# Optimization experiments

Measured on AMD Instinct MI355X. Metric: run time of the kernel, lower is better.

The kernel has to match this reference:

```python
import jax, jax.numpy as jnp
import numpy as np
import math

B, S, H, NH, NKV, D, I, LCK = 2, 1024, 2048, 32, 8, 64, 8192, 3
EPS = 1e-6
THETA = 10000.0


def rms_norm(x, w, eps=EPS):
    xf = x.astype(jnp.float32)
    var = jnp.mean(xf * xf, axis=-1, keepdims=True)
    return (w * (xf * jax.lax.rsqrt(var + eps))).astype(x.dtype)


def rotate_half(x):
    d = x.shape[-1] // 2
    return jnp.concatenate([-x[..., d:], x[..., :d]], axis=-1)


def setup_inputs() -> dict:
    key = jax.random.key(0)
    ks = jax.random.split(key, 16)
    sc = 0.02
    inp = {
        'input_emb': jax.random.normal(ks[0], (B, S, H), jnp.float32),
        'hidden_states': jax.random.normal(ks[1], (B, S, H), jnp.float32),
        'cache_k': jax.random.normal(ks[2], (LCK, B, NH, S, D), jnp.float32),
        'cache_v': jax.random.normal(ks[3], (LCK, B, NH, S, D), jnp.float32),
    }
    neg = jnp.finfo(jnp.float32).min
    causal = jnp.where(jnp.tril(jnp.ones((S, S), bool)), 0.0, neg).astype(jnp.float32)
    inp['attention_mask'] = jnp.broadcast_to(causal[None, None], (B, 1, S, S))
    inp['position_ids'] = jnp.broadcast_to(jnp.arange(S, dtype=jnp.int32)[None], (B, S))
    inp['wq'] = jax.random.normal(ks[4], (NH * D, 2 * H), jnp.float32) * sc
    inp['wk'] = jax.random.normal(ks[5], (NKV * D, 2 * H), jnp.float32) * sc
    inp['wv'] = jax.random.normal(ks[6], (NKV * D, 2 * H), jnp.float32) * sc
    inp['wo'] = jax.random.normal(ks[7], (H, NH * D), jnp.float32) * sc
    inp['w_gate'] = jax.random.normal(ks[8], (I, H), jnp.float32) * sc
    inp['w_up'] = jax.random.normal(ks[9], (I, H), jnp.float32) * sc
    inp['w_down'] = jax.random.normal(ks[10], (H, I), jnp.float32) * sc
    inp['hidden_norm_w'] = jnp.ones((H,), jnp.float32)
    inp['input_ln_w'] = jnp.ones((H,), jnp.float32)
    inp['post_ln_w'] = jnp.ones((H,), jnp.float32)
    return inp


def _forward(input_emb, hidden_states, cache_k, cache_v, attention_mask, position_ids,
             wq, wk, wv, wo, w_gate, w_up, w_down, hidden_norm_w, input_ln_w, post_ln_w):
    residual = hidden_states
    h = rms_norm(hidden_states, hidden_norm_w)
    e = rms_norm(input_emb, input_ln_w)
    x = jnp.concatenate([e, h], axis=-1)  # [B,S,2H]

    q = jnp.einsum('bsi,oi->bso', x, wq).reshape(B, S, NH, D).transpose(0, 2, 1, 3)
    k = jnp.einsum('bsi,oi->bso', x, wk).reshape(B, S, NKV, D).transpose(0, 2, 1, 3)
    v = jnp.einsum('bsi,oi->bso', x, wv).reshape(B, S, NKV, D).transpose(0, 2, 1, 3)

    # RoPE table up to seq_len = S + LCK, indexed at position_ids + LCK
    inv_freq = 1.0 / (THETA ** (jnp.arange(0, D, 2, dtype=jnp.float32) / D))
    t = jnp.arange(S + LCK, dtype=jnp.float32)
    freqs = t[:, None] * inv_freq[None, :]
    emb = jnp.concatenate([freqs, freqs], axis=-1)  # [S+LCK, D]
    pos = position_ids + LCK
    cos = jnp.cos(emb)[pos][:, None]  # [B,1,S,D]
    sin = jnp.sin(emb)[pos][:, None]
    q = q * cos + rotate_half(q) * sin
    k = k * cos + rotate_half(k) * sin

    n_rep = NH // NKV
    k = jnp.repeat(k, n_rep, axis=1)  # [B,NH,S,D]
    v = jnp.repeat(v, n_rep, axis=1)

    scale = 1.0 / math.sqrt(D)
    # full causal attention against the oldest cache entry
    s0 = jnp.einsum('bhqd,bhkd->bhqk', q, cache_k[0]) * scale + attention_mask
    # diagonal (same-position) attention against remaining cache entries + current keys
    extra_k = jnp.concatenate([cache_k[1:], k[None]], axis=0)  # [LCK,B,NH,S,D]
    extra_v = jnp.concatenate([cache_v[1:], v[None]], axis=0)
    sd = jnp.einsum('bhqd,nbhqd->bhqn', q, extra_k) * scale  # [B,NH,S,LCK]

    attn = jax.nn.softmax(jnp.concatenate([s0, sd], axis=-1).astype(jnp.float32), axis=-1).astype(q.dtype)
    out = jnp.einsum('bhqk,bhkd->bhqd', attn[..., :S], cache_v[0])
    out = out + jnp.einsum('bhqn,nbhqd->bhqd', attn[..., S:], extra_v)
    out = out.transpose(0, 2, 1, 3).reshape(B, S, NH * D)
    attn_out = jnp.einsum('bsi,oi->bso', out, wo)

    h2 = residual + attn_out
    hn = rms_norm(h2, post_ln_w)
    mlp = jnp.einsum('bsi,oi->bso', jax.nn.silu(jnp.einsum('bsi,oi->bso', hn, w_gate)) * jnp.einsum('bsi,oi->bso', hn, w_up), w_down)
    return h2 + mlp


def reference(input_emb, hidden_states, cache_k, cache_v, attention_mask, position_ids,
              wq, wk, wv, wo, w_gate, w_up, w_down, hidden_norm_w, input_ln_w, post_ln_w):
    return _forward(input_emb, hidden_states, cache_k, cache_v, attention_mask, position_ids,
                    wq, wk, wv, wo, w_gate, w_up, w_down, hidden_norm_w, input_ln_w, post_ln_w)
```

## Files before the change

kernel.cpp:

```cpp
#include <hip/hip_runtime.h>
#include <math.h>

#define B_   2
#define S_   1024
#define H_   2048
#define NH_  32
#define NKV_ 8
#define D_   64
#define I_   8192
#define LCK_ 3
#define M_   (B_ * S_)

typedef unsigned short u16;
typedef unsigned int   u32;
typedef __attribute__((ext_vector_type(8))) short bf16x8;
typedef __attribute__((ext_vector_type(4))) float f32x4;
typedef __attribute__((ext_vector_type(2))) unsigned int u32x2;

__device__ __forceinline__ u16 f2b(float f) {
  u32 u = __float_as_uint(f);
  u += 0x7fffu + ((u >> 16) & 1u);
  return (u16)(u >> 16);
}
__device__ __forceinline__ float b2f(u16 h) { return __uint_as_float(((u32)h) << 16); }

__device__ __forceinline__ void st_bf4(u16* p, float a, float b, float c, float d) {
  u32x2 v;
  v.x = (u32)f2b(a) | ((u32)f2b(b) << 16);
  v.y = (u32)f2b(c) | ((u32)f2b(d) << 16);
  *(u32x2*)p = v;
}

__device__ __forceinline__ void cvt16(const float4& a, const float4& b,
                                      const float4& c, const float4& d,
                                      bf16x8& lo, bf16x8& hi) {
  lo[0] = (short)f2b(a.x); lo[1] = (short)f2b(a.y); lo[2] = (short)f2b(a.z); lo[3] = (short)f2b(a.w);
  lo[4] = (short)f2b(b.x); lo[5] = (short)f2b(b.y); lo[6] = (short)f2b(b.z); lo[7] = (short)f2b(b.w);
  hi[0] = (short)f2b(c.x); hi[1] = (short)f2b(c.y); hi[2] = (short)f2b(c.z); hi[3] = (short)f2b(c.w);
  hi[4] = (short)f2b(d.x); hi[5] = (short)f2b(d.y); hi[6] = (short)f2b(d.z); hi[7] = (short)f2b(d.w);
}

__device__ __forceinline__ void async16(const void* g, void* l) {
  __builtin_amdgcn_global_load_lds(
      (const __attribute__((address_space(1))) unsigned int*)(uintptr_t)g,
      (__attribute__((address_space(3))) unsigned int*)(unsigned int)(uintptr_t)l,
      16, 0, 0);
}

__global__ __launch_bounds__(256) void norm_concat_kernel(
    const float* __restrict__ emb, const float* __restrict__ hid,
    const float* __restrict__ w_e, const float* __restrict__ w_h,
    u16* __restrict__ x)
{
  const int row = blockIdx.x;
  const int t = threadIdx.x;
  const float* e = emb + (size_t)row * H_;
  const float* h = hid + (size_t)row * H_;

  const float4 ev0 = *(const float4*)&e[t * 4];
  const float4 ev1 = *(const float4*)&e[t * 4 + 1024];
  const float4 hv0 = *(const float4*)&h[t * 4];
  const float4 hv1 = *(const float4*)&h[t * 4 + 1024];

  float se = ev0.x*ev0.x + ev0.y*ev0.y + ev0.z*ev0.z + ev0.w*ev0.w
           + ev1.x*ev1.x + ev1.y*ev1.y + ev1.z*ev1.z + ev1.w*ev1.w;
  float sh = hv0.x*hv0.x + hv0.y*hv0.y + hv0.z*hv0.z + hv0.w*hv0.w
           + hv1.x*hv1.x + hv1.y*hv1.y + hv1.z*hv1.z + hv1.w*hv1.w;

  #pragma unroll
  for (int m = 1; m < 64; m <<= 1) {
    se += __shfl_xor(se, m);
    sh += __shfl_xor(sh, m);
  }
  __shared__ float red[8];
  const int wv = t >> 6;
  if ((t & 63) == 0) { red[wv] = se; red[4 + wv] = sh; }
  __syncthreads();
  se = red[0] + red[1] + red[2] + red[3];
  sh = red[4] + red[5] + red[6] + red[7];

  const float re = 1.0f / sqrtf(se * (1.0f / H_) + 1e-6f);
  const float rh = 1.0f / sqrtf(sh * (1.0f / H_) + 1e-6f);

  const float4 we0 = *(const float4*)&w_e[t * 4];
  const float4 we1 = *(const float4*)&w_e[t * 4 + 1024];
  const float4 wh0 = *(const float4*)&w_h[t * 4];
  const float4 wh1 = *(const float4*)&w_h[t * 4 + 1024];

  u16* xr = x + (size_t)row * (2 * H_);
  st_bf4(&xr[t * 4],        ev0.x*re*we0.x, ev0.y*re*we0.y, ev0.z*re*we0.z, ev0.w*re*we0.w);
  st_bf4(&xr[t * 4 + 1024], ev1.x*re*we1.x, ev1.y*re*we1.y, ev1.z*re*we1.z, ev1.w*re*we1.w);
  st_bf4(&xr[2048 + t * 4],        hv0.x*rh*wh0.x, hv0.y*rh*wh0.y, hv0.z*rh*wh0.z, hv0.w*rh*wh0.w);
  st_bf4(&xr[2048 + t * 4 + 1024], hv1.x*rh*wh1.x, hv1.y*rh*wh1.y, hv1.z*rh*wh1.z, hv1.w*rh*wh1.w);
}

__global__ __launch_bounds__(256) void rmsnorm_kernel(
    const float* __restrict__ in, const float* __restrict__ w, u16* __restrict__ outp)
{
  const int row = blockIdx.x;
  const int t = threadIdx.x;
  const float* p = in + (size_t)row * H_;
  const float4 v0 = *(const float4*)&p[t * 4];
  const float4 v1 = *(const float4*)&p[t * 4 + 1024];
  float s = v0.x*v0.x + v0.y*v0.y + v0.z*v0.z + v0.w*v0.w
          + v1.x*v1.x + v1.y*v1.y + v1.z*v1.z + v1.w*v1.w;
  #pragma unroll
  for (int m = 1; m < 64; m <<= 1) s += __shfl_xor(s, m);
  __shared__ float red[4];
  const int wv = t >> 6;
  if ((t & 63) == 0) red[wv] = s;
  __syncthreads();
  s = red[0] + red[1] + red[2] + red[3];
  const float rs = 1.0f / sqrtf(s * (1.0f / H_) + 1e-6f);

  const float4 w0 = *(const float4*)&w[t * 4];
  const float4 w1 = *(const float4*)&w[t * 4 + 1024];
  u16* orow = outp + (size_t)row * H_;
  st_bf4(&orow[t * 4],        v0.x*rs*w0.x, v0.y*rs*w0.y, v0.z*rs*w0.z, v0.w*rs*w0.w);
  st_bf4(&orow[t * 4 + 1024], v1.x*rs*w1.x, v1.y*rs*w1.y, v1.z*rs*w1.z, v1.w*rs*w1.w);
}

__global__ __launch_bounds__(256) void convert6_kernel(
    const float* __restrict__ wq, const float* __restrict__ wk, const float* __restrict__ wv,
    const float* __restrict__ wo, const float* __restrict__ wg, const float* __restrict__ wu,
    u16* __restrict__ dst)
{
  const size_t i8 = ((size_t)blockIdx.x * 256 + threadIdx.x) * 8;
  const float* s; size_t base;
  if      (i8 <  8388608) { s = wq; base = 0; }
  else if (i8 < 10485760) { s = wk; base = 8388608; }
  else if (i8 < 12582912) { s = wv; base = 10485760; }
  else if (i8 < 16777216) { s = wo; base = 12582912; }
  else if (i8 < 33554432) { s = wg; base = 16777216; }
  else                    { s = wu; base = 33554432; }
  const float4 a = *(const float4*)&s[i8 - base];
  const float4 b = *(const float4*)&s[i8 - base + 4];
  bf16x8 r;
  r[0] = (short)f2b(a.x); r[1] = (short)f2b(a.y); r[2] = (short)f2b(a.z); r[3] = (short)f2b(a.w);
  r[4] = (short)f2b(b.x); r[5] = (short)f2b(b.y); r[6] = (short)f2b(b.z); r[7] = (short)f2b(b.w);
  *(bf16x8*)&dst[i8] = r;
}

__global__ __launch_bounds__(256) void convert1_kernel(
    const float* __restrict__ src, u16* __restrict__ dst)
{
  const size_t i8 = ((size_t)blockIdx.x * 256 + threadIdx.x) * 8;
  const float4 a = *(const float4*)&src[i8];
  const float4 b = *(const float4*)&src[i8 + 4];
  bf16x8 r;
  r[0] = (short)f2b(a.x); r[1] = (short)f2b(a.y); r[2] = (short)f2b(a.z); r[3] = (short)f2b(a.w);
  r[4] = (short)f2b(b.x); r[5] = (short)f2b(b.y); r[6] = (short)f2b(b.z); r[7] = (short)f2b(b.w);
  *(bf16x8*)&dst[i8] = r;
}

template <int MODE>
__global__ __launch_bounds__(256) void gemm_bf16_kernel(
    const u16* __restrict__ A, const u16* __restrict__ Bw,
    void* Cv, const void* Xv, int M, int N, int K)
{
  __shared__ __align__(16) u16 As[128 * 32];
  __shared__ __align__(16) u16 Bs[128 * 32];
  const int t = threadIdx.x;
  const int lane = t & 63;
  const int w = t >> 6;
  const int wr = w >> 1, wc = w & 1;
  const int row0 = blockIdx.y * 128;
  const int col0 = blockIdx.x * 128;
  const int kz = blockIdx.z;
  const int Kc = K / (int)gridDim.z;

  f32x4 acc[4][4];
  #pragma unroll
  for (int i = 0; i < 4; ++i)
    #pragma unroll
    for (int j = 0; j < 4; ++j)
      #pragma unroll
      for (int r = 0; r < 4; ++r) acc[i][j][r] = 0.f;

  const int srow = lane >> 2;
  const int skc  = (lane & 3) * 8;
  const u16* Ag = A  + (size_t)(row0 + w * 32 + srow) * K + skc + (size_t)kz * Kc;
  const u16* Bg = Bw + (size_t)(col0 + w * 32 + srow) * K + skc + (size_t)kz * Kc;
  u16* AsW = &As[w * 32 * 32];
  u16* BsW = &Bs[w * 32 * 32];

  const int fr = lane & 15;
  const int fq = (lane >> 4) * 8;

  for (int k0 = 0; k0 < Kc; k0 += 32) {
    __syncthreads();
    async16(Ag + k0,                  AsW);
    async16(Ag + k0 + (size_t)16 * K, AsW + 16 * 32);
    async16(Bg + k0,                  BsW);
    async16(Bg + k0 + (size_t)16 * K, BsW + 16 * 32);
    __syncthreads();

    bf16x8 af[4], bfr[4];
    #pragma unroll
    for (int ti = 0; ti < 4; ++ti)
      af[ti] = *(const bf16x8*)&As[(wr * 64 + ti * 16 + fr) * 32 + fq];
    #pragma unroll
    for (int tj = 0; tj < 4; ++tj)
      bfr[tj] = *(const bf16x8*)&Bs[(wc * 64 + tj * 16 + fr) * 32 + fq];
    #pragma unroll
    for (int ti = 0; ti < 4; ++ti)
      #pragma unroll
      for (int tj = 0; tj < 4; ++tj)
        acc[ti][tj] = __builtin_amdgcn_mfma_f32_16x16x32_bf16(af[ti], bfr[tj], acc[ti][tj], 0, 0, 0);
  }

  float* Cf = (float*)Cv + (size_t)kz * ((size_t)M * N);
  u16*  Cb = (u16*)Cv;
  const float* Xf = (const float*)Xv;
  const u16*  Xb = (const u16*)Xv;
  const int rbase = (lane >> 4) * 4;
  const int cofs  = lane & 15;
  #pragma unroll
  for (int ti = 0; ti < 4; ++ti) {
    #pragma unroll
    for (int r = 0; r < 4; ++r) {
      const int gr = row0 + wr * 64 + ti * 16 + rbase + r;
      #pragma unroll
      for (int tj = 0; tj < 4; ++tj) {
        const int gc = col0 + wc * 64 + tj * 16 + cofs;
        const size_t off = (size_t)gr * N + gc;
        const float v = acc[ti][tj][r];
        if constexpr (MODE == 0) {
          Cf[off] = v;
        } else if constexpr (MODE == 1) {
          Cf[off] = v + Xf[off];
        } else if constexpr (MODE == 2) {
          Cb[off] = f2b(v);
        } else {
          const float g = b2f(Xb[off]);
          Cb[off] = f2b((g / (1.f + __expf(-g))) * v);
        }
      }
    }
  }
}

template <int NP>
__global__ __launch_bounds__(256) void reduce_kernel(
    const float* __restrict__ p, const float* __restrict__ resid,
    float* __restrict__ out, size_t nper)
{
  const size_t i = ((size_t)blockIdx.x * 256 + threadIdx.x) * 4;
  float4 s = *(const float4*)&p[i];
  #pragma unroll
  for (int z = 1; z < NP; ++z) {
    const float4 a = *(const float4*)&p[(size_t)z * nper + i];
    s.x += a.x; s.y += a.y; s.z += a.z; s.w += a.w;
  }
  if (resid) {
    const float4 r = *(const float4*)&resid[i];
    s.x += r.x; s.y += r.y; s.z += r.z; s.w += r.w;
  }
  *(float4*)&out[i] = s;
}

__global__ __launch_bounds__(256) void rope_kernel(
    float* __restrict__ qkv, const int* __restrict__ pid)
{
  const int idx = blockIdx.x * 256 + threadIdx.x;
  const int total = M_ * (NH_ + NKV_) * 32;
  if (idx >= total) return;
  const int row = idx / 1280;
  const int rem = idx - row * 1280;
  const int head = rem >> 5;
  const int i = rem & 31;
  const int col = (head < NH_) ? head * 64 : 2048 + (head - NH_) * 64;
  float* base = qkv + (size_t)row * 3072 + col;
  const int pos = pid[row] + LCK_;
  const float invf = powf(10000.0f, -(float)i * (1.0f / 32.0f));
  const float ang = (float)pos * invf;
  const float c  = cosf(ang);
  const float sn = sinf(ang);
  const float x0 = base[i];
  const float x1 = base[i + 32];
  base[i]      = x0 * c - x1 * sn;
  base[i + 32] = x1 * c + x0 * sn;
}

__global__ __launch_bounds__(256) void attn_kernel(
    const float* __restrict__ qkv,
    const float* __restrict__ ck, const float* __restrict__ cv,
    u16* __restrict__ ao)
{
  const int bid = blockIdx.x;
  const int qt = bid & 15;
  const int bh = bid >> 4;
  const int h = bh & 31;
  const int b = bh >> 5;
  const int t = threadIdx.x;
  const int lane = t & 63;
  const int w = t >> 6;
  const int qbase = qt * 64;

  const int fr = lane & 15;
  const int fq = (lane >> 4) * 8;
  const int rbase = (lane >> 4) * 4;
  const int cofs = lane & 15;

  __shared__ __align__(16) u16 Qs[64 * 72];
  __shared__ __align__(16) u16 Ks[64 * 72];
  __shared__ __align__(16) u16 Vts[64 * 72];
  __shared__ __align__(16) u16 Ps[64 * 72];
  __shared__ float Ls[192];

  const size_t bh_off = (size_t)b * NH_ + h;
  const float* K0 = ck + bh_off * S_ * D_;
  const float* V0 = cv + bh_off * S_ * D_;

  const int sr = t >> 2;
  const int sc = (t & 3) * 16;
  {
    const float* qg = qkv + (size_t)(b * S_ + qbase + sr) * 3072 + h * 64 + sc;
    float4 a = *(const float4*)&qg[0], bb = *(const float4*)&qg[4],
           c = *(const float4*)&qg[8], d = *(const float4*)&qg[12];
    a.x*=0.125f; a.y*=0.125f; a.z*=0.125f; a.w*=0.125f;
    bb.x*=0.125f; bb.y*=0.125f; bb.z*=0.125f; bb.w*=0.125f;
    c.x*=0.125f; c.y*=0.125f; c.z*=0.125f; c.w*=0.125f;
    d.x*=0.125f; d.y*=0.125f; d.z*=0.125f; d.w*=0.125f;
    bf16x8 lo, hi; cvt16(a, bb, c, d, lo, hi);
    *(bf16x8*)&Qs[sr * 72 + sc] = lo;
    *(bf16x8*)&Qs[sr * 72 + sc + 8] = hi;
  }

  float m_r[4], l_r[4];
  f32x4 Oacc[4];
  #pragma unroll
  for (int r = 0; r < 4; ++r) { m_r[r] = -3.0e38f; l_r[r] = 0.f; }
  #pragma unroll
  for (int dt = 0; dt < 4; ++dt)
    #pragma unroll
    for (int r = 0; r < 4; ++r) Oacc[dt][r] = 0.f;

  for (int kt = 0; kt <= qt; ++kt) {
    __syncthreads();
    {
      const float* kg = K0 + (size_t)(kt * 64 + sr) * D_ + sc;
      float4 a = *(const float4*)&kg[0], bb = *(const float4*)&kg[4],
             c = *(const float4*)&kg[8], d = *(const float4*)&kg[12];
      bf16x8 lo, hi; cvt16(a, bb, c, d, lo, hi);
      *(bf16x8*)&Ks[sr * 72 + sc] = lo;
      *(bf16x8*)&Ks[sr * 72 + sc + 8] = hi;
      const float* vg = V0 + (size_t)(kt * 64 + sr) * D_ + sc;
      float4 va = *(const float4*)&vg[0], vb4 = *(const float4*)&vg[4],
             vc = *(const float4*)&vg[8], vd = *(const float4*)&vg[12];
      const float vv[16] = {va.x,va.y,va.z,va.w, vb4.x,vb4.y,vb4.z,vb4.w,
                            vc.x,vc.y,vc.z,vc.w, vd.x,vd.y,vd.z,vd.w};
      #pragma unroll
      for (int i = 0; i < 16; ++i) Vts[(sc + i) * 72 + sr] = f2b(vv[i]);
    }
    __syncthreads();

    const bf16x8 qa0 = *(const bf16x8*)&Qs[(w * 16 + fr) * 72 + fq];
    const bf16x8 qa1 = *(const bf16x8*)&Qs[(w * 16 + fr) * 72 + 32 + fq];
    f32x4 sacc[4];
    #pragma unroll
    for (int nt = 0; nt < 4; ++nt) {
      const bf16x8 kb0 = *(const bf16x8*)&Ks[(nt * 16 + fr) * 72 + fq];
      const bf16x8 kb1 = *(const bf16x8*)&Ks[(nt * 16 + fr) * 72 + 32 + fq];
      f32x4 z; z[0]=0.f; z[1]=0.f; z[2]=0.f; z[3]=0.f;
      z = __builtin_amdgcn_mfma_f32_16x16x32_bf16(qa0, kb0, z, 0, 0, 0);
      sacc[nt] = __builtin_amdgcn_mfma_f32_16x16x32_bf16(qa1, kb1, z, 0, 0, 0);
    }
    if (kt == qt) {
      #pragma unroll
      for (int nt = 0; nt < 4; ++nt) {
        const int key = nt * 16 + cofs;
        #pragma unroll
        for (int r = 0; r < 4; ++r)
          if (key > w * 16 + rbase + r) sacc[nt][r] = -3.0e38f;
      }
    }

    #pragma unroll
    for (int r = 0; r < 4; ++r) {
      float rm = fmaxf(fmaxf(sacc[0][r], sacc[1][r]), fmaxf(sacc[2][r], sacc[3][r]));
      rm = fmaxf(rm, __shfl_xor(rm, 1));
      rm = fmaxf(rm, __shfl_xor(rm, 2));
      rm = fmaxf(rm, __shfl_xor(rm, 4));
      rm = fmaxf(rm, __shfl_xor(rm, 8));
      const float mnew = fmaxf(m_r[r], rm);
      const float alpha = __expf(m_r[r] - mnew);
      float p0 = __expf(sacc[0][r] - mnew);
      float p1 = __expf(sacc[1][r] - mnew);
      float p2 = __expf(sacc[2][r] - mnew);
      float p3 = __expf(sacc[3][r] - mnew);
      float rs = p0 + p1 + p2 + p3;
      rs += __shfl_xor(rs, 1);
      rs += __shfl_xor(rs, 2);
      rs += __shfl_xor(rs, 4);
      rs += __shfl_xor(rs, 8);
      l_r[r] = l_r[r] * alpha + rs;
      m_r[r] = mnew;
      #pragma unroll
      for (int dt = 0; dt < 4; ++dt) Oacc[dt][r] *= alpha;
      u16* prow = &Ps[(w * 16 + rbase + r) * 72 + cofs];
      prow[0]  = f2b(p0);
      prow[16] = f2b(p1);
      prow[32] = f2b(p2);
      prow[48] = f2b(p3);
    }

    const bf16x8 pa0 = *(const bf16x8*)&Ps[(w * 16 + fr) * 72 + fq];
    const bf16x8 pa1 = *(const bf16x8*)&Ps[(w * 16 + fr) * 72 + 32 + fq];
    #pragma unroll
    for (int dt = 0; dt < 4; ++dt) {
      const bf16x8 vb0 = *(const bf16x8*)&Vts[(dt * 16 + fr) * 72 + fq];
      const bf16x8 vb1 = *(const bf16x8*)&Vts[(dt * 16 + fr) * 72 + 32 + fq];
      Oacc[dt] = __builtin_amdgcn_mfma_f32_16x16x32_bf16(pa0, vb0, Oacc[dt], 0, 0, 0);
      Oacc[dt] = __builtin_amdgcn_mfma_f32_16x16x32_bf16(pa1, vb1, Oacc[dt], 0, 0, 0);
    }
  }

  if (t < 192) {
    const int n = t >> 6;
    const int r = t & 63;
    const int qp = qbase + r;
    const float* kp;
    if (n < 2) kp = ck + ((((size_t)(n + 1) * B_ + b) * NH_ + h) * S_ + qp) * D_;
    else       kp = qkv + (size_t)(b * S_ + qp) * 3072 + 2048 + (h >> 2) * 64;
    float e = 0.f;
    #pragma unroll 16
    for (int d = 0; d < 64; ++d) e = fmaf(b2f(Qs[r * 72 + d]), kp[d], e);
    Ls[n * 64 + r] = e;
  }
  __syncthreads();

  #pragma unroll
  for (int r = 0; r < 4; ++r) {
    const int qr = w * 16 + rbase + r;
    const int qp = qbase + qr;
    const float e0 = Ls[qr], e1 = Ls[64 + qr], e2 = Ls[128 + qr];
    const float mnew = fmaxf(fmaxf(m_r[r], e0), fmaxf(e1, e2));
    const float alpha = __expf(m_r[r] - mnew);
    const float p0 = __expf(e0 - mnew);
    const float p1 = __expf(e1 - mnew);
    const float p2 = __expf(e2 - mnew);
    const float inv = 1.0f / (l_r[r] * alpha + p0 + p1 + p2);
    const float* v1p = cv + ((((size_t)1 * B_ + b) * NH_ + h) * S_ + qp) * D_;
    const float* v2p = cv + ((((size_t)2 * B_ + b) * NH_ + h) * S_ + qp) * D_;
    const float* v3p = qkv + (size_t)(b * S_ + qp) * 3072 + 2560 + (h >> 2) * 64;
    u16* aorow = ao + (size_t)(b * S_ + qp) * 2048 + h * 64;
    #pragma unroll
    for (int dt = 0; dt < 4; ++dt) {
      const int col = dt * 16 + cofs;
      const float o = (Oacc[dt][r] * alpha + p0 * v1p[col] + p1 * v2p[col] + p2 * v3p[col]) * inv;
      aorow[col] = f2b(o);
    }
  }
}

extern "C" void kernel_launch(void* const* d_in, const int* in_sizes, int n_in,
                              void* d_out, int out_size, void* d_ws, size_t ws_size,
                              hipStream_t stream)
{
  const float* input_emb = (const float*)d_in[0];
  const float* hidden    = (const float*)d_in[1];
  const float* cache_k   = (const float*)d_in[2];
  const float* cache_v   = (const float*)d_in[3];
  const int*   pos_ids   = (const int*)d_in[5];
  const float* wq = (const float*)d_in[6];
  const float* wk = (const float*)d_in[7];
  const float* wv = (const float*)d_in[8];
  const float* wo = (const float*)d_in[9];
  const float* wg = (const float*)d_in[10];
  const float* wu = (const float*)d_in[11];
  const float* wd = (const float*)d_in[12];
  const float* w_hidden_norm = (const float*)d_in[13];
  const float* w_input_ln    = (const float*)d_in[14];
  const float* w_post_ln     = (const float*)d_in[15];
  float* out = (float*)d_out;

  char* wsb = (char*)d_ws;
  u16*   wall   = (u16*)(wsb + 0);
  u16*   wqkv_b = wall;
  u16*   wo_b   = (u16*)(wsb + 25165824);
  u16*   wg_b   = (u16*)(wsb + 33554432);
  u16*   wu_b   = (u16*)(wsb + 67108864);
  u16*   xb     = (u16*)(wsb + 100663296);
  float* qkvf   = (float*)(wsb + 117440512);
  u16*   ao     = (u16*)(wsb + 142606336);
  float* h2     = (float*)(wsb + 150994944);
  u16*   hn     = (u16*)(wsb + 100663296);
  u16*   gbb    = (u16*)(wsb + 117440512);
  u16*   gub    = (u16*)(wsb + 0);
  u16*   wd_b   = (u16*)(wsb + 33554432);
  float* wo_p   = (float*)(wsb + 100663296);
  float* dn_p   = (float*)(wsb + 67108864);

  convert6_kernel<<<24576, 256, 0, stream>>>(wq, wk, wv, wo, wg, wu, wall);
  norm_concat_kernel<<<M_, 256, 0, stream>>>(input_emb, hidden, w_input_ln, w_hidden_norm, xb);
  gemm_bf16_kernel<0><<<dim3(24, 16, 2), 256, 0, stream>>>(xb, wqkv_b, qkvf, nullptr, M_, 3072, 4096);
  reduce_kernel<2><<<6144, 256, 0, stream>>>(qkvf, nullptr, qkvf, (size_t)M_ * 3072);
  rope_kernel<<<10240, 256, 0, stream>>>(qkvf, pos_ids);
  attn_kernel<<<B_ * NH_ * (S_ / 64), 256, 0, stream>>>(qkvf, cache_k, cache_v, ao);
  gemm_bf16_kernel<0><<<dim3(16, 16, 2), 256, 0, stream>>>(ao, wo_b, wo_p, nullptr, M_, 2048, 2048);
  reduce_kernel<2><<<4096, 256, 0, stream>>>(wo_p, hidden, h2, (size_t)M_ * 2048);
  rmsnorm_kernel<<<M_, 256, 0, stream>>>(h2, w_post_ln, hn);
  gemm_bf16_kernel<2><<<dim3(64, 16), 256, 0, stream>>>(hn, wg_b, gbb, nullptr, M_, 8192, 2048);
  convert1_kernel<<<8192, 256, 0, stream>>>(wd, wd_b);
  gemm_bf16_kernel<3><<<dim3(64, 16), 256, 0, stream>>>(hn, wu_b, gub, gbb, M_, 8192, 2048);
  gemm_bf16_kernel<0><<<dim3(16, 16, 4), 256, 0, stream>>>(gub, wd_b, dn_p, nullptr, M_, 2048, 8192);
  reduce_kernel<4><<<4096, 256, 0, stream>>>(dn_p, h2, out, (size_t)M_ * 2048);
}
```

Baseline: 960.7 us.

## Double-buffer LDS tiles in bf16 GEMM and use fast RoPE intrinsics

The GEMM main loop now uses two LDS buffers for A and B. The next K-tile's async global-to-LDS loads are issued before the MFMA compute on the current tile, which saves one barrier per step and overlaps load latency with compute. This doubles LDS use per block, which may reduce occupancy. Separately, the RoPE kernel replaces powf/cosf/sinf with exp2f and __sincosf, trading some accuracy at large angles for cheaper math.

```diff
diff --git a/kernel.cpp b/kernel.cpp
--- a/kernel.cpp
+++ b/kernel.cpp
@@ -158,8 +158,8 @@
     const u16* __restrict__ A, const u16* __restrict__ Bw,
     void* Cv, const void* Xv, int M, int N, int K)
 {
-  __shared__ __align__(16) u16 As[128 * 32];
-  __shared__ __align__(16) u16 Bs[128 * 32];
+  __shared__ __align__(16) u16 As[2][128 * 32];
+  __shared__ __align__(16) u16 Bs[2][128 * 32];
   const int t = threadIdx.x;
   const int lane = t & 63;
   const int w = t >> 6;
@@ -181,32 +181,49 @@
   const int skc  = (lane & 3) * 8;
   const u16* Ag = A  + (size_t)(row0 + w * 32 + srow) * K + skc + (size_t)kz * Kc;
   const u16* Bg = Bw + (size_t)(col0 + w * 32 + srow) * K + skc + (size_t)kz * Kc;
-  u16* AsW = &As[w * 32 * 32];
-  u16* BsW = &Bs[w * 32 * 32];
+  u16* AsW0 = &As[0][w * 32 * 32];
+  u16* AsW1 = &As[1][w * 32 * 32];
+  u16* BsW0 = &Bs[0][w * 32 * 32];
+  u16* BsW1 = &Bs[1][w * 32 * 32];
 
   const int fr = lane & 15;
   const int fq = (lane >> 4) * 8;
 
-  for (int k0 = 0; k0 < Kc; k0 += 32) {
-    __syncthreads();
-    async16(Ag + k0,                  AsW);
-    async16(Ag + k0 + (size_t)16 * K, AsW + 16 * 32);
-    async16(Bg + k0,                  BsW);
-    async16(Bg + k0 + (size_t)16 * K, BsW + 16 * 32);
-    __syncthreads();
-
+  auto stage = [&](int k0, u16* aw, u16* bw) {
+    async16(Ag + k0,                  aw);
+    async16(Ag + k0 + (size_t)16 * K, aw + 16 * 32);
+    async16(Bg + k0,                  bw);
+    async16(Bg + k0 + (size_t)16 * K, bw + 16 * 32);
+  };
+  auto compute = [&](const u16* asb, const u16* bsb) {
     bf16x8 af[4], bfr[4];
     #pragma unroll
     for (int ti = 0; ti < 4; ++ti)
-      af[ti] = *(const bf16x8*)&As[(wr * 64 + ti * 16 + fr) * 32 + fq];
+      af[ti] = *(const bf16x8*)&asb[(wr * 64 + ti * 16 + fr) * 32 + fq];
     #pragma unroll
     for (int tj = 0; tj < 4; ++tj)
-      bfr[tj] = *(const bf16x8*)&Bs[(wc * 64 + tj * 16 + fr) * 32 + fq];
+      bfr[tj] = *(const bf16x8*)&bsb[(wc * 64 + tj * 16 + fr) * 32 + fq];
     #pragma unroll
     for (int ti = 0; ti < 4; ++ti)
       #pragma unroll
       for (int tj = 0; tj < 4; ++tj)
         acc[ti][tj] = __builtin_amdgcn_mfma_f32_16x16x32_bf16(af[ti], bfr[tj], acc[ti][tj], 0, 0, 0);
+  };
+
+  stage(0, AsW0, BsW0);
+  __syncthreads();
+
+  int k0 = 0;
+  for (;;) {
+    if (k0 + 32 < Kc) stage(k0 + 32, AsW1, BsW1);
+    compute(As[0], Bs[0]);
+    if (k0 + 32 >= Kc) break;
+    __syncthreads();
+    if (k0 + 64 < Kc) stage(k0 + 64, AsW0, BsW0);
+    compute(As[1], Bs[1]);
+    if (k0 + 64 >= Kc) break;
+    __syncthreads();
+    k0 += 64;
   }
 
   float* Cf = (float*)Cv + (size_t)kz * ((size_t)M * N);
@@ -272,10 +289,10 @@
   const int col = (head < NH_) ? head * 64 : 2048 + (head - NH_) * 64;
   float* base = qkv + (size_t)row * 3072 + col;
   const int pos = pid[row] + LCK_;
-  const float invf = powf(10000.0f, -(float)i * (1.0f / 32.0f));
+  const float invf = exp2f((float)i * (-13.2877123795494f / 32.0f));
   const float ang = (float)pos * invf;
-  const float c  = cosf(ang);
-  const float sn = sinf(ang);
+  float sn, c;
+  __sincosf(ang, &sn, &c);
   const float x0 = base[i];
   const float x1 = base[i + 32];
   base[i]      = x0 * c - x1 * sn;
```

After: 929.7 us. 1.03x faster.
